# Optimization experiments

Measured on AMD Instinct MI355X. Metric: run time of the kernel, lower is better.

The kernel has to match this reference:

```python
import jax, jax.numpy as jnp
import numpy as np

BATCH_SIZE = 64
SEQ = 150           # hardcoded 150 in the original module
N = BATCH_SIZE * SEQ  # 9600
D = 128             # feature dim of h_real
K = 16              # n_clusters


def setup_inputs() -> dict:
    key = jax.random.key(0)
    k1, k2 = jax.random.split(key)
    h_real = jax.random.normal(k1, (N, D), dtype=jnp.float32)
    # torch.nn.init.orthogonal_ on an [N, K] tall matrix -> column-orthonormal via QR
    F_raw = jax.random.normal(k2, (N, K), dtype=jnp.float32)
    F, _ = jnp.linalg.qr(F_raw)
    return {"h_real": h_real, "F": F}


def reference(h_real, F):
    # Original: WTW = h h^T (NxN); loss = trace(WTW) - trace(F^T WTW F).
    # Same math without the NxN Gram matrix:
    #   trace(h h^T) = sum(h * h)
    #   trace(F^T h h^T F) = ||h^T F||_F^2
    tr_wtw = jnp.sum(h_real * h_real)
    M = jnp.einsum('nd,nk->dk', h_real, F)  # [D, K]
    tr_fwtwf = jnp.sum(M * M)
    return tr_wtw - tr_fwtwf
```

## Files before the change

kernel.cpp:

```cpp
#include <hip/hip_runtime.h>


#define GA 240

__global__ __launch_bounds__(256) void kmeans_partial(
    const float* __restrict__ h, const float* __restrict__ F,
    float* __restrict__ ws, int N) {
    const int t  = threadIdx.x;
    const int k  = t & 15;
    const int dg = t >> 4;

    float acc[8] = {0.f, 0.f, 0.f, 0.f, 0.f, 0.f, 0.f, 0.f};
    float ssq = 0.f;

    for (int n = blockIdx.x; n < N; n += gridDim.x) {
        const float f = F[n * 16 + k];
        const float4* hrow = reinterpret_cast<const float4*>(h + n * 128) + dg * 2;
        const float4 a = hrow[0];
        const float4 b = hrow[1];
        acc[0] += a.x * f; acc[1] += a.y * f; acc[2] += a.z * f; acc[3] += a.w * f;
        acc[4] += b.x * f; acc[5] += b.y * f; acc[6] += b.z * f; acc[7] += b.w * f;
        if (k == 0) {
            ssq += a.x * a.x + a.y * a.y + a.z * a.z + a.w * a.w
                 + b.x * b.x + b.y * b.y + b.z * b.z + b.w * b.w;
        }
    }

    const int d0 = dg * 8;
    #pragma unroll
    for (int j = 0; j < 8; ++j) {
        atomicAdd(&ws[(d0 + j) * 16 + k], acc[j]);
    }

    #pragma unroll
    for (int off = 32; off > 0; off >>= 1) {
        ssq += __shfl_down(ssq, off);
    }
    if ((t & 63) == 0) {
        atomicAdd(&ws[2048], ssq);
    }
}

__global__ __launch_bounds__(256) void kmeans_finish(
    const float* __restrict__ ws, float* __restrict__ out) {
    const int t = threadIdx.x;
    float s = 0.f;
    #pragma unroll
    for (int j = 0; j < 8; ++j) {
        const float m = ws[t * 8 + j];
        s += m * m;
    }
    #pragma unroll
    for (int off = 32; off > 0; off >>= 1) {
        s += __shfl_down(s, off);
    }
    __shared__ float red[4];
    if ((t & 63) == 0) red[t >> 6] = s;
    __syncthreads();
    if (t == 0) {
        const float sm2 = red[0] + red[1] + red[2] + red[3];
        out[0] = ws[2048] - sm2;
    }
}

extern "C" void kernel_launch(void* const* d_in, const int* in_sizes, int n_in,
                              void* d_out, int out_size, void* d_ws, size_t ws_size,
                              hipStream_t stream) {
    const float* h = (const float*)d_in[0];
    const float* F = (const float*)d_in[1];
    float* out = (float*)d_out;
    float* ws  = (float*)d_ws;

    const int N = in_sizes[0] / 128;

    hipMemsetAsync(ws, 0, 2049 * sizeof(float), stream);

    kmeans_partial<<<GA, 256, 0, stream>>>(h, F, ws, N);
    kmeans_finish<<<1, 256, 0, stream>>>(ws, out);
}
```

Measured before the change: 86.05 us.

## Fuse partial and finish kernels with last-block reduction and larger blocks

```diff
diff --git a/kernel.cpp b/kernel.cpp
--- a/kernel.cpp
+++ b/kernel.cpp
@@ -1,23 +1,35 @@
 #include <hip/hip_runtime.h>
 
 
-#define GA 240
+#define NROWS        9600
+#define BLOCKS       240
+#define ROWS_PER_BLK (NROWS / BLOCKS)
+#define ROWS_PER_TM  (ROWS_PER_BLK / 4)
 
-__global__ __launch_bounds__(256) void kmeans_partial(
+__global__ __launch_bounds__(1024) void kmeans_fused(
     const float* __restrict__ h, const float* __restrict__ F,
-    float* __restrict__ ws, int N) {
-    const int t  = threadIdx.x;
-    const int k  = t & 15;
-    const int dg = t >> 4;
+    float* __restrict__ ws, float* __restrict__ out, int nrows) {
 
-    float acc[8] = {0.f, 0.f, 0.f, 0.f, 0.f, 0.f, 0.f, 0.f};
+    const int t   = threadIdx.x;
+    const int tm  = t >> 8;
+    const int tid = t & 255;
+    const int k   = tid & 15;
+    const int dg  = tid >> 4;
+
+    const int row0 = blockIdx.x * ROWS_PER_BLK + tm * ROWS_PER_TM;
+
+    float acc[8] = {0.f,0.f,0.f,0.f,0.f,0.f,0.f,0.f};
     float ssq = 0.f;
 
-    for (int n = blockIdx.x; n < N; n += gridDim.x) {
-        const float f = F[n * 16 + k];
-        const float4* hrow = reinterpret_cast<const float4*>(h + n * 128) + dg * 2;
-        const float4 a = hrow[0];
-        const float4 b = hrow[1];
+    const float4* hb = reinterpret_cast<const float4*>(h);
+
+    #pragma unroll 2
+    for (int r = 0; r < ROWS_PER_TM; ++r) {
+        const int n = row0 + r;
+        if (n >= nrows) break;
+        const float  f = F[n * 16 + k];
+        const float4 a = hb[n * 32 + dg * 2 + 0];
+        const float4 b = hb[n * 32 + dg * 2 + 1];
         acc[0] += a.x * f; acc[1] += a.y * f; acc[2] += a.z * f; acc[3] += a.w * f;
         acc[4] += b.x * f; acc[5] += b.y * f; acc[6] += b.z * f; acc[7] += b.w * f;
         if (k == 0) {
@@ -26,40 +38,62 @@
         }
     }
 
-    const int d0 = dg * 8;
-    #pragma unroll
-    for (int j = 0; j < 8; ++j) {
-        atomicAdd(&ws[(d0 + j) * 16 + k], acc[j]);
+    __shared__ float part[3][2048];
+    __shared__ float ssq_part[64];
+
+    if (tm > 0) {
+        #pragma unroll
+        for (int j = 0; j < 8; ++j)
+            part[tm - 1][dg * 128 + j * 16 + k] = acc[j];
+    }
+    if (k == 0) ssq_part[t >> 4] = ssq;
+    __syncthreads();
+
+    if (tm == 0) {
+        #pragma unroll
+        for (int j = 0; j < 8; ++j) {
+            const int c = dg * 128 + j * 16 + k;
+            atomicAdd(&ws[c], acc[j] + part[0][c] + part[1][c] + part[2][c]);
+        }
+    }
+    if (t < 64) {
+        float s = ssq_part[t];
+        #pragma unroll
+        for (int off = 32; off; off >>= 1) s += __shfl_down(s, off);
+        if (t == 0) atomicAdd(&ws[2048], s);
     }
 
-    #pragma unroll
-    for (int off = 32; off > 0; off >>= 1) {
-        ssq += __shfl_down(ssq, off);
+    __shared__ bool is_last;
+    __threadfence();
+    __syncthreads();
+    if (t == 0) {
+        unsigned prev = __hip_atomic_fetch_add(
+            reinterpret_cast<unsigned*>(&ws[2049]), 1u,
+            __ATOMIC_ACQ_REL, __HIP_MEMORY_SCOPE_AGENT);
+        is_last = (prev == (unsigned)(gridDim.x - 1));
     }
-    if ((t & 63) == 0) {
-        atomicAdd(&ws[2048], ssq);
-    }
-}
+    __syncthreads();
+    if (!is_last) return;
 
-__global__ __launch_bounds__(256) void kmeans_finish(
-    const float* __restrict__ ws, float* __restrict__ out) {
-    const int t = threadIdx.x;
     float s = 0.f;
     #pragma unroll
-    for (int j = 0; j < 8; ++j) {
-        const float m = ws[t * 8 + j];
+    for (int c = t; c < 2048; c += 1024) {
+        const float m = __hip_atomic_load(&ws[c], __ATOMIC_RELAXED,
+                                          __HIP_MEMORY_SCOPE_AGENT);
         s += m * m;
     }
     #pragma unroll
-    for (int off = 32; off > 0; off >>= 1) {
-        s += __shfl_down(s, off);
-    }
-    __shared__ float red[4];
+    for (int off = 32; off; off >>= 1) s += __shfl_down(s, off);
+    __shared__ float red[16];
     if ((t & 63) == 0) red[t >> 6] = s;
     __syncthreads();
     if (t == 0) {
-        const float sm2 = red[0] + red[1] + red[2] + red[3];
-        out[0] = ws[2048] - sm2;
+        float sm2 = 0.f;
+        #pragma unroll
+        for (int i = 0; i < 16; ++i) sm2 += red[i];
+        const float ssq_tot = __hip_atomic_load(&ws[2048], __ATOMIC_RELAXED,
+                                                __HIP_MEMORY_SCOPE_AGENT);
+        out[0] = ssq_tot - sm2;
     }
 }
 
@@ -71,10 +105,9 @@
     float* out = (float*)d_out;
     float* ws  = (float*)d_ws;
 
-    const int N = in_sizes[0] / 128;
+    const int nrows = in_sizes[0] >> 7;
 
-    hipMemsetAsync(ws, 0, 2049 * sizeof(float), stream);
+    hipMemsetAsync(ws, 0, 2056 * sizeof(float), stream);
 
-    kmeans_partial<<<GA, 256, 0, stream>>>(h, F, ws, N);
-    kmeans_finish<<<1, 256, 0, stream>>>(ws, out);
+    kmeans_fused<<<BLOCKS, 1024, 0, stream>>>(h, F, ws, out, nrows);
 }
```

Result: slower. 119.7 us (+39.1%).

## Replace global atomics and memset with per-block shared-memory partials

Applied to the files above, without the earlier changes.

```diff
diff --git a/kernel.cpp b/kernel.cpp
--- a/kernel.cpp
+++ b/kernel.cpp
@@ -1,23 +1,37 @@
 #include <hip/hip_runtime.h>
 
 
-#define GA 240
+#define BLOCKS1  48
+#define SSQ_OFF  (BLOCKS1 * 2048)
 
-__global__ __launch_bounds__(256) void kmeans_partial(
+__global__ __launch_bounds__(1024) void kmeans_part1(
     const float* __restrict__ h, const float* __restrict__ F,
-    float* __restrict__ ws, int N) {
-    const int t  = threadIdx.x;
-    const int k  = t & 15;
-    const int dg = t >> 4;
+    float* __restrict__ ws, int nrows) {
 
-    float acc[8] = {0.f, 0.f, 0.f, 0.f, 0.f, 0.f, 0.f, 0.f};
+    const int t   = threadIdx.x;
+    const int tm  = t >> 8;
+    const int tid = t & 255;
+    const int k   = tid & 15;
+    const int dg  = tid >> 4;
+
+    const int rpb   = (nrows + BLOCKS1 - 1) / BLOCKS1;
+    const int rpt   = (rpb + 3) >> 2;
+    const int bbase = blockIdx.x * rpb;
+    const int row0  = bbase + tm * rpt;
+    int rowend = row0 + rpt;
+    if (rowend > bbase + rpb) rowend = bbase + rpb;
+    if (rowend > nrows)       rowend = nrows;
+
+    float acc[8] = {0.f,0.f,0.f,0.f,0.f,0.f,0.f,0.f};
     float ssq = 0.f;
 
-    for (int n = blockIdx.x; n < N; n += gridDim.x) {
-        const float f = F[n * 16 + k];
-        const float4* hrow = reinterpret_cast<const float4*>(h + n * 128) + dg * 2;
-        const float4 a = hrow[0];
-        const float4 b = hrow[1];
+    const float4* hb = reinterpret_cast<const float4*>(h);
+
+    #pragma unroll 5
+    for (int n = row0; n < rowend; ++n) {
+        const float  f = F[(n << 4) + k];
+        const float4 a = hb[(n << 5) + (dg << 1) + 0];
+        const float4 b = hb[(n << 5) + (dg << 1) + 1];
         acc[0] += a.x * f; acc[1] += a.y * f; acc[2] += a.z * f; acc[3] += a.w * f;
         acc[4] += b.x * f; acc[5] += b.y * f; acc[6] += b.z * f; acc[7] += b.w * f;
         if (k == 0) {
@@ -26,40 +40,62 @@
         }
     }
 
-    const int d0 = dg * 8;
-    #pragma unroll
-    for (int j = 0; j < 8; ++j) {
-        atomicAdd(&ws[(d0 + j) * 16 + k], acc[j]);
-    }
+    __shared__ float part[4][2048];
+    __shared__ float ssqp[16];
 
     #pragma unroll
-    for (int off = 32; off > 0; off >>= 1) {
-        ssq += __shfl_down(ssq, off);
-    }
-    if ((t & 63) == 0) {
-        atomicAdd(&ws[2048], ssq);
+    for (int j = 0; j < 8; ++j)
+        part[tm][(dg << 7) + (((j + dg) & 7) << 4) + k] = acc[j];
+
+    #pragma unroll
+    for (int off = 32; off; off >>= 1) ssq += __shfl_down(ssq, off);
+    if ((t & 63) == 0) ssqp[t >> 6] = ssq;
+    __syncthreads();
+
+    const float2* p2 = reinterpret_cast<const float2*>(part);
+    const float2 a2 = p2[         t];
+    const float2 b2 = p2[1024  +  t];
+    const float2 c2 = p2[2048  +  t];
+    const float2 d2 = p2[3072  +  t];
+    float2 o;
+    o.x = a2.x + b2.x + c2.x + d2.x;
+    o.y = a2.y + b2.y + c2.y + d2.y;
+    reinterpret_cast<float2*>(ws)[(blockIdx.x << 10) + t] = o;
+
+    if (t == 0) {
+        float sq = 0.f;
+        #pragma unroll
+        for (int i = 0; i < 16; ++i) sq += ssqp[i];
+        ws[SSQ_OFF + blockIdx.x] = sq;
     }
 }
 
-__global__ __launch_bounds__(256) void kmeans_finish(
+__global__ __launch_bounds__(512) void kmeans_part2(
     const float* __restrict__ ws, float* __restrict__ out) {
+
     const int t = threadIdx.x;
-    float s = 0.f;
+    const float4* A = reinterpret_cast<const float4*>(ws);
+
+    float4 m = make_float4(0.f, 0.f, 0.f, 0.f);
+    #pragma unroll 8
+    for (int b = 0; b < BLOCKS1; ++b) {
+        const float4 v = A[(b << 9) + t];
+        m.x += v.x; m.y += v.y; m.z += v.z; m.w += v.w;
+    }
+    float s = m.x * m.x + m.y * m.y + m.z * m.z + m.w * m.w;
+
     #pragma unroll
-    for (int j = 0; j < 8; ++j) {
-        const float m = ws[t * 8 + j];
-        s += m * m;
-    }
-    #pragma unroll
-    for (int off = 32; off > 0; off >>= 1) {
-        s += __shfl_down(s, off);
-    }
-    __shared__ float red[4];
+    for (int off = 32; off; off >>= 1) s += __shfl_down(s, off);
+    __shared__ float red[8];
     if ((t & 63) == 0) red[t >> 6] = s;
     __syncthreads();
-    if (t == 0) {
-        const float sm2 = red[0] + red[1] + red[2] + red[3];
-        out[0] = ws[2048] - sm2;
+
+    if (t < 64) {
+        float v = (t < BLOCKS1) ? ws[SSQ_OFF + t] : 0.f;
+        if (t < 8) v -= red[t];
+        #pragma unroll
+        for (int off = 32; off; off >>= 1) v += __shfl_down(v, off);
+        if (t == 0) out[0] = v;
     }
 }
 
@@ -71,10 +107,8 @@
     float* out = (float*)d_out;
     float* ws  = (float*)d_ws;
 
-    const int N = in_sizes[0] / 128;
+    const int nrows = in_sizes[0] >> 7;
 
-    hipMemsetAsync(ws, 0, 2049 * sizeof(float), stream);
-
-    kmeans_partial<<<GA, 256, 0, stream>>>(h, F, ws, N);
-    kmeans_finish<<<1, 256, 0, stream>>>(ws, out);
+    kmeans_part1<<<BLOCKS1, 1024, 0, stream>>>(h, F, ws, nrows);
+    kmeans_part2<<<1, 512, 0, stream>>>(ws, out);
 }
```

Measured after the change: 80.72 us, median of 2. 6.2% less time.
